# Kernel optimization log

Measured on AMD Instinct MI355X. Metric: run time of the kernel, lower is better.

Reference implementation:

```python
import jax, jax.numpy as jnp
import numpy as np

NUM_NUM = 32    # numerical (pass-through) features
NUM_CAT = 32    # embedded categorical features
CARD = 128      # one-hot width per categorical feature
OUT = 32        # per-feature embedding output dim (0.25 * 128)
BATCH = 16384


def setup_inputs() -> dict:
    key = jax.random.key(0)
    k1, k2, k3 = jax.random.split(key, 3)
    x = jax.random.normal(k1, (BATCH, NUM_NUM + NUM_CAT * CARD), dtype=jnp.float32)
    # stacked per-feature nn.Linear(CARD, OUT) weights/biases (all same shape)
    W = jax.random.normal(k2, (NUM_CAT, CARD, OUT), dtype=jnp.float32) / np.sqrt(CARD).astype(np.float32)
    b = jax.random.normal(k3, (NUM_CAT, OUT), dtype=jnp.float32) * 0.01
    return {"x": x, "W": W, "b": b}


def reference(x, W, b):
    # Numerical columns pass through unchanged; each categorical one-hot slice
    # goes through its own small Linear, then everything is concatenated.
    # Since all categorical slices have identical width, the per-feature loop of
    # small GEMMs is expressed as one batched (block-diagonal) matmul.
    x_num = x[..., :NUM_NUM]                                      # [B, 32]
    x_cat = x[..., NUM_NUM:].reshape(x.shape[:-1] + (NUM_CAT, CARD))  # [B, F, C]
    emb = jnp.einsum('bfc,fco->bfo', x_cat, W) + b                # [B, F, OUT]
    emb = emb.reshape(x.shape[:-1] + (NUM_CAT * OUT,))            # [B, 1024]
    return jnp.concatenate([x_num, emb], axis=-1)                 # [B, 1056]
```

## Files before the change

kernel.cpp:

```cpp
#include <hip/hip_runtime.h>
#include <stdint.h>

#define BATCH   16384
#define NUM_NUM 32
#define NUM_CAT 32
#define CARD    128
#define OUT_F   32
#define XSTRIDE 4128
#define OSTRIDE 1056

typedef __attribute__((ext_vector_type(8))) short short8;
typedef __attribute__((ext_vector_type(4))) float f32x4;

__device__ __forceinline__ unsigned short f2bf(float f) {
    unsigned u = __builtin_bit_cast(unsigned, f);
    return (unsigned short)((u + 0x7FFFu + ((u >> 16) & 1u)) >> 16);
}

__global__ __launch_bounds__(256, 4) void emb_mfma(const float* __restrict__ x,
                                                   const float* __restrict__ Wm,
                                                   const float* __restrict__ bias,
                                                   float* __restrict__ out) {
    const int f    = blockIdx.x;
    const int row0 = blockIdx.y * 256;
    const int tid  = threadIdx.x;
    const int l    = tid & 63;
    const int wv   = tid >> 6;
    const int lr   = l & 15;
    const int lg   = l >> 4;

    const float* wf = Wm + (size_t)f * (CARD * OUT_F);
    short8 bw[2][4];
#pragma unroll
    for (int n = 0; n < 2; ++n)
#pragma unroll
        for (int kf = 0; kf < 4; ++kf)
#pragma unroll
            for (int i = 0; i < 8; ++i)
                bw[n][kf][i] = (short)f2bf(wf[(kf * 32 + lg * 8 + i) * OUT_F + n * 16 + lr]);

    const float bias0 = bias[f * OUT_F + lr];
    const float bias1 = bias[f * OUT_F + 16 + lr];

    const float* xf    = x + NUM_NUM + f * CARD;
    float*       obase = out + NUM_NUM + f * OUT_F;
    const int    wrow  = row0 + wv * 64;

    float4 v[2][8];

    {
        const float* xr = xf + (size_t)(wrow + lr) * XSTRIDE;
#pragma unroll
        for (int kf = 0; kf < 4; ++kf) {
            v[0][kf * 2]     = *(const float4*)(xr + kf * 32 + lg * 8);
            v[0][kf * 2 + 1] = *(const float4*)(xr + kf * 32 + lg * 8 + 4);
        }
    }

#pragma unroll
    for (int m = 0; m < 4; ++m) {
        if (m < 3) {
            const float* xr = xf + (size_t)(wrow + (m + 1) * 16 + lr) * XSTRIDE;
#pragma unroll
            for (int kf = 0; kf < 4; ++kf) {
                v[(m + 1) & 1][kf * 2]     = *(const float4*)(xr + kf * 32 + lg * 8);
                v[(m + 1) & 1][kf * 2 + 1] = *(const float4*)(xr + kf * 32 + lg * 8 + 4);
            }
        }

        f32x4 acc0 = {0.f, 0.f, 0.f, 0.f};
        f32x4 acc1 = {0.f, 0.f, 0.f, 0.f};
#pragma unroll
        for (int kf = 0; kf < 4; ++kf) {
            const float4 v0 = v[m & 1][kf * 2];
            const float4 v1 = v[m & 1][kf * 2 + 1];
            short8       af;
            af[0] = (short)f2bf(v0.x); af[1] = (short)f2bf(v0.y);
            af[2] = (short)f2bf(v0.z); af[3] = (short)f2bf(v0.w);
            af[4] = (short)f2bf(v1.x); af[5] = (short)f2bf(v1.y);
            af[6] = (short)f2bf(v1.z); af[7] = (short)f2bf(v1.w);
            acc0 = __builtin_amdgcn_mfma_f32_16x16x32_bf16(af, bw[0][kf], acc0, 0, 0, 0);
            acc1 = __builtin_amdgcn_mfma_f32_16x16x32_bf16(af, bw[1][kf], acc1, 0, 0, 0);
        }

#pragma unroll
        for (int r = 0; r < 4; ++r) {
            const size_t orow = (size_t)(wrow + m * 16 + lg * 4 + r) * OSTRIDE;
            obase[orow + lr]      = acc0[r] + bias0;
            obase[orow + 16 + lr] = acc1[r] + bias1;
        }
    }

    if (f == (blockIdx.y & 31)) {
        const float4* src = (const float4*)(x + (size_t)(row0 + tid) * XSTRIDE);
        float4*       dst = (float4*)(out + (size_t)(row0 + tid) * OSTRIDE);
#pragma unroll
        for (int q = 0; q < 8; ++q) dst[q] = src[q];
    }
}

extern "C" void kernel_launch(void* const* d_in, const int* in_sizes, int n_in,
                              void* d_out, int out_size, void* d_ws, size_t ws_size,
                              hipStream_t stream) {
    const float* x    = (const float*)d_in[0];
    const float* W    = (const float*)d_in[1];
    const float* bias = (const float*)d_in[2];
    float*       out  = (float*)d_out;

    dim3 grid(NUM_CAT, BATCH / 256);
    emb_mfma<<<grid, 256, 0, stream>>>(x, W, bias, out);
}
```

Baseline: 80.12 us.

## Process feature pairs per block with waves split across rows and output halves

Each block now handles two adjacent categorical features over 128 rows instead of one feature over 256 rows. Waves split into two row halves and two 16-column output halves, so each wave reads a contiguous 256-float span per row (two features) and holds weights for both features. The goal is longer contiguous global reads per row and better DRAM locality. In exchange, the cross-iteration prefetch double-buffer is removed, each A fragment is converted to bf16 twice by different waves (the row data is loaded redundantly by the two nh waves), and the grid shape changes.

```diff
diff --git a/kernel.cpp b/kernel.cpp
--- a/kernel.cpp
+++ b/kernel.cpp
@@ -17,85 +17,91 @@
     return (unsigned short)((u + 0x7FFFu + ((u >> 16) & 1u)) >> 16);
 }
 
-__global__ __launch_bounds__(256, 4) void emb_mfma(const float* __restrict__ x,
+__global__ __launch_bounds__(256, 4) void emb_pair(const float* __restrict__ x,
                                                    const float* __restrict__ Wm,
                                                    const float* __restrict__ bias,
                                                    float* __restrict__ out) {
-    const int f    = blockIdx.x;
-    const int row0 = blockIdx.y * 256;
-    const int tid  = threadIdx.x;
-    const int l    = tid & 63;
-    const int wv   = tid >> 6;
-    const int lr   = l & 15;
-    const int lg   = l >> 4;
+    const int p     = blockIdx.x;
+    const int row0  = blockIdx.y * 128;
+    const int tid   = threadIdx.x;
+    const int l     = tid & 63;
+    const int wv    = tid >> 6;
+    const int rhalf = wv & 1;
+    const int nh    = wv >> 1;
+    const int lr    = l & 15;
+    const int lg    = l >> 4;
 
-    const float* wf = Wm + (size_t)f * (CARD * OUT_F);
     short8 bw[2][4];
 #pragma unroll
-    for (int n = 0; n < 2; ++n)
+    for (int ff = 0; ff < 2; ++ff) {
+        const float* wf = Wm + (size_t)(p * 2 + ff) * (CARD * OUT_F);
 #pragma unroll
         for (int kf = 0; kf < 4; ++kf)
 #pragma unroll
             for (int i = 0; i < 8; ++i)
-                bw[n][kf][i] = (short)f2bf(wf[(kf * 32 + lg * 8 + i) * OUT_F + n * 16 + lr]);
+                bw[ff][kf][i] =
+                    (short)f2bf(wf[(kf * 32 + lg * 8 + i) * OUT_F + nh * 16 + lr]);
+    }
 
-    const float bias0 = bias[f * OUT_F + lr];
-    const float bias1 = bias[f * OUT_F + 16 + lr];
+    const float bias0 = bias[(p * 2 + 0) * OUT_F + nh * 16 + lr];
+    const float bias1 = bias[(p * 2 + 1) * OUT_F + nh * 16 + lr];
 
-    const float* xf    = x + NUM_NUM + f * CARD;
-    float*       obase = out + NUM_NUM + f * OUT_F;
-    const int    wrow  = row0 + wv * 64;
-
-    float4 v[2][8];
-
-    {
-        const float* xr = xf + (size_t)(wrow + lr) * XSTRIDE;
-#pragma unroll
-        for (int kf = 0; kf < 4; ++kf) {
-            v[0][kf * 2]     = *(const float4*)(xr + kf * 32 + lg * 8);
-            v[0][kf * 2 + 1] = *(const float4*)(xr + kf * 32 + lg * 8 + 4);
-        }
-    }
+    const float* xp    = x + NUM_NUM + p * 256;
+    float*       obase = out + NUM_NUM + p * 2 * OUT_F + nh * 16;
+    const int    wrow  = row0 + rhalf * 64;
 
 #pragma unroll
     for (int m = 0; m < 4; ++m) {
-        if (m < 3) {
-            const float* xr = xf + (size_t)(wrow + (m + 1) * 16 + lr) * XSTRIDE;
+        const float* xr = xp + (size_t)(wrow + m * 16 + lr) * XSTRIDE;
+
+        float4 v0[8], v1[8];
 #pragma unroll
-            for (int kf = 0; kf < 4; ++kf) {
-                v[(m + 1) & 1][kf * 2]     = *(const float4*)(xr + kf * 32 + lg * 8);
-                v[(m + 1) & 1][kf * 2 + 1] = *(const float4*)(xr + kf * 32 + lg * 8 + 4);
-            }
+        for (int kf = 0; kf < 4; ++kf) {
+            v0[kf * 2]     = *(const float4*)(xr + kf * 32 + lg * 8);
+            v0[kf * 2 + 1] = *(const float4*)(xr + kf * 32 + lg * 8 + 4);
+        }
+#pragma unroll
+        for (int kf = 0; kf < 4; ++kf) {
+            v1[kf * 2]     = *(const float4*)(xr + 128 + kf * 32 + lg * 8);
+            v1[kf * 2 + 1] = *(const float4*)(xr + 128 + kf * 32 + lg * 8 + 4);
         }
 
         f32x4 acc0 = {0.f, 0.f, 0.f, 0.f};
         f32x4 acc1 = {0.f, 0.f, 0.f, 0.f};
 #pragma unroll
         for (int kf = 0; kf < 4; ++kf) {
-            const float4 v0 = v[m & 1][kf * 2];
-            const float4 v1 = v[m & 1][kf * 2 + 1];
-            short8       af;
-            af[0] = (short)f2bf(v0.x); af[1] = (short)f2bf(v0.y);
-            af[2] = (short)f2bf(v0.z); af[3] = (short)f2bf(v0.w);
-            af[4] = (short)f2bf(v1.x); af[5] = (short)f2bf(v1.y);
-            af[6] = (short)f2bf(v1.z); af[7] = (short)f2bf(v1.w);
+            short8 af;
+            af[0] = (short)f2bf(v0[kf * 2].x);     af[1] = (short)f2bf(v0[kf * 2].y);
+            af[2] = (short)f2bf(v0[kf * 2].z);     af[3] = (short)f2bf(v0[kf * 2].w);
+            af[4] = (short)f2bf(v0[kf * 2 + 1].x); af[5] = (short)f2bf(v0[kf * 2 + 1].y);
+            af[6] = (short)f2bf(v0[kf * 2 + 1].z); af[7] = (short)f2bf(v0[kf * 2 + 1].w);
             acc0 = __builtin_amdgcn_mfma_f32_16x16x32_bf16(af, bw[0][kf], acc0, 0, 0, 0);
+        }
+#pragma unroll
+        for (int kf = 0; kf < 4; ++kf) {
+            short8 af;
+            af[0] = (short)f2bf(v1[kf * 2].x);     af[1] = (short)f2bf(v1[kf * 2].y);
+            af[2] = (short)f2bf(v1[kf * 2].z);     af[3] = (short)f2bf(v1[kf * 2].w);
+            af[4] = (short)f2bf(v1[kf * 2 + 1].x); af[5] = (short)f2bf(v1[kf * 2 + 1].y);
+            af[6] = (short)f2bf(v1[kf * 2 + 1].z); af[7] = (short)f2bf(v1[kf * 2 + 1].w);
             acc1 = __builtin_amdgcn_mfma_f32_16x16x32_bf16(af, bw[1][kf], acc1, 0, 0, 0);
         }
 
 #pragma unroll
         for (int r = 0; r < 4; ++r) {
             const size_t orow = (size_t)(wrow + m * 16 + lg * 4 + r) * OSTRIDE;
-            obase[orow + lr]      = acc0[r] + bias0;
-            obase[orow + 16 + lr] = acc1[r] + bias1;
+            obase[orow + lr]          = acc0[r] + bias0;
+            obase[orow + OUT_F + lr]  = acc1[r] + bias1;
         }
     }
 
-    if (f == (blockIdx.y & 31)) {
-        const float4* src = (const float4*)(x + (size_t)(row0 + tid) * XSTRIDE);
-        float4*       dst = (float4*)(out + (size_t)(row0 + tid) * OSTRIDE);
+    if (p == (blockIdx.y & 15)) {
+        const int r    = tid >> 1;
+        const int half = (tid & 1) * 16;
+        const float4* src = (const float4*)(x + (size_t)(row0 + r) * XSTRIDE + half);
+        float4*       dst = (float4*)(out + (size_t)(row0 + r) * OSTRIDE + half);
 #pragma unroll
-        for (int q = 0; q < 8; ++q) dst[q] = src[q];
+        for (int q = 0; q < 4; ++q) dst[q] = src[q];
     }
 }
 
@@ -107,6 +113,6 @@
     const float* bias = (const float*)d_in[2];
     float*       out  = (float*)d_out;
 
-    dim3 grid(NUM_CAT, BATCH / 256);
-    emb_mfma<<<grid, 256, 0, stream>>>(x, W, bias, out);
+    dim3 grid(NUM_CAT / 2, BATCH / 128);
+    emb_pair<<<grid, 256, 0, stream>>>(x, W, bias, out);
 }
```

Result: slower. 96.26 us (+20.1%).
